# Optimization experiments

Measured on AMD Instinct MI355X. Metric: run time of the kernel, lower is better.

The kernel has to match this reference:

```python
import jax, jax.numpy as jnp
import numpy as np

N = 50000      # nodes
E = 625000     # directed edges
F_IN, H1, H2, OUT = 128, 128, 64, 50


def setup_inputs() -> dict:
    key = jax.random.key(0)
    ks = jax.random.split(key, 5)
    x = jax.random.normal(ks[0], (N, F_IN), dtype=jnp.float32)
    edge_index = jax.random.randint(ks[1], (2, E), 0, N, dtype=jnp.int64)
    W1 = jax.random.normal(ks[2], (F_IN, H1), dtype=jnp.float32) * 0.05
    b1 = jnp.zeros((H1,), jnp.float32)
    W2 = jax.random.normal(ks[3], (H1, H2), dtype=jnp.float32) * 0.05
    b2 = jnp.zeros((H2,), jnp.float32)
    Wh = jax.random.normal(ks[4], (H2, OUT), dtype=jnp.float32) * 0.05
    bh = jnp.zeros((OUT,), jnp.float32)
    return {"x": x, "edge_index": edge_index, "W1": W1, "b1": b1,
            "W2": W2, "b2": b2, "Wh": Wh, "bh": bh}


def _gcn_conv(h, W, b, src, dst, dinv, n):
    # h' = D^{-1/2} A_hat D^{-1/2} (h W) + b, A_hat includes self-loops
    h = h @ W                                   # [n, out]
    coef = (dinv[src] * dinv[dst])[:, None]      # [e, 1]
    agg = jax.ops.segment_sum(h[src] * coef, dst, num_segments=n)
    return agg + b


def reference(x, edge_index, W1, b1, W2, b2, Wh, bh):
    n = x.shape[0]
    loops = jnp.arange(n, dtype=edge_index.dtype)
    src = jnp.concatenate([edge_index[0], loops])
    dst = jnp.concatenate([edge_index[1], loops])
    # symmetric GCN normalization: deg over destinations (incl. self-loops)
    deg = jax.ops.segment_sum(jnp.ones(src.shape[0], x.dtype), dst, num_segments=n)
    dinv = jnp.where(deg > 0, jax.lax.rsqrt(deg), 0.0)
    # dropout is a no-op in eval mode (training=False)
    h = _gcn_conv(x, W1, b1, src, dst, dinv, n)
    h = jax.nn.relu(h)
    h = _gcn_conv(h, W2, b2, src, dst, dinv, n)
    h = jax.nn.relu(h)
    return h @ Wh + bh
```

## Files before the change

### kernel.cpp

```cpp
#include <hip/hip_runtime.h>

#define F_IN 128
#define HH1 128
#define HH2 64
#define FOUT 50
#define EB 256
#define NBUCK_MAX 256

typedef __attribute__((ext_vector_type(8))) short short8;
typedef __attribute__((ext_vector_type(4))) short s16x4;
typedef __attribute__((ext_vector_type(4))) float f32x4;

__device__ inline short f2bf(float f) {
    union { float f; unsigned u; } v; v.f = f;
    unsigned r = v.u + 0x7fffu + ((v.u >> 16) & 1u);
    return (short)(r >> 16);
}
__device__ inline float bf2f(short s) {
    union { float f; unsigned u; } v; v.u = ((unsigned)(unsigned short)s) << 16;
    return v.f;
}

__device__ inline int detect64(const unsigned* raw) {
    __shared__ int s_is64;
    if (threadIdx.x == 0) s_is64 = 1;
    __syncthreads();
    if (raw[2 * threadIdx.x + 1] != 0u) atomicAnd(&s_is64, 0);
    __syncthreads();
    return s_is64;
}

__global__ __launch_bounds__(256) void bucket_count(
    const int* __restrict__ raw, int E, int nbuck, int* __restrict__ parthist,
    const float* __restrict__ W1, const float* __restrict__ W2,
    const float* __restrict__ Wh, short* __restrict__ W1t,
    short* __restrict__ W2t, short* __restrict__ Wht) {
    __shared__ int hist[NBUCK_MAX];
    const int tid = threadIdx.x;
    int is64 = detect64((const unsigned*)raw);
    for (int k = tid; k < nbuck; k += 256) hist[k] = 0;
    __syncthreads();
    const int CH = (E + EB - 1) / EB;
    const int e0 = blockIdx.x * CH, e1 = min(E, e0 + CH);
    for (int e = e0 + tid; e < e1; e += 256) {
        int d = is64 ? raw[2 * (long)E + 2 * e] : raw[E + e];
        atomicAdd(&hist[d >> 8], 1);
    }
    __syncthreads();
    for (int k = tid; k < nbuck; k += 256) parthist[blockIdx.x * nbuck + k] = hist[k];
    const int T1 = HH1 * F_IN, T2 = HH2 * HH1, T3 = 64 * HH2;
    int idx = blockIdx.x * 256 + tid;
    if (idx < T1) {
        int c = idx / F_IN, k = idx - c * F_IN;
        W1t[idx] = f2bf(W1[(long)k * HH1 + c]);
    } else if (idx < T1 + T2) {
        int i = idx - T1;
        int c = i / HH1, k = i - c * HH1;
        W2t[i] = f2bf(W2[(long)k * HH2 + c]);
    } else if (idx < T1 + T2 + T3) {
        int i = idx - T1 - T2;
        int c = i / HH2, k = i - c * HH2;
        Wht[i] = f2bf((c < FOUT) ? Wh[(long)k * FOUT + c] : 0.f);
    }
}

__global__ __launch_bounds__(256) void bucket_scan(
    int* __restrict__ parthist, int* __restrict__ bbase, int nbuck, int E) {
    __shared__ int sh[256];
    const int k = threadIdx.x;
    int sum = 0;
    if (k < nbuck)
        for (int b = 0; b < EB; ++b) sum += parthist[b * nbuck + k];
    int v = (k < nbuck) ? sum : 0;
    sh[k] = v;
    __syncthreads();
    for (int off = 1; off < 256; off <<= 1) {
        int t = (k >= off) ? sh[k - off] : 0;
        __syncthreads();
        sh[k] += t;
        __syncthreads();
    }
    int base = sh[k] - v;
    if (k < nbuck) bbase[k] = base;
    if (k == 0) bbase[nbuck] = E;
    if (k < nbuck) {
        int run = base;
        for (int b = 0; b < EB; ++b) {
            int t = parthist[b * nbuck + k];
            parthist[b * nbuck + k] = run;
            run += t;
        }
    }
}

__global__ __launch_bounds__(256) void scatter_gemm1(
    const int* __restrict__ raw, int E, int nbuck,
    const int* __restrict__ parthist, int2* __restrict__ tmp,
    const float* __restrict__ x, const short* __restrict__ W1t,
    short* __restrict__ h1, int n) {
    const int tid = threadIdx.x;
    if (blockIdx.x < EB) {
        __shared__ int cur[NBUCK_MAX];
        int is64 = detect64((const unsigned*)raw);
        for (int k = tid; k < nbuck; k += 256) cur[k] = parthist[blockIdx.x * nbuck + k];
        __syncthreads();
        const int CH = (E + EB - 1) / EB;
        const int e0 = blockIdx.x * CH, e1 = min(E, e0 + CH);
        for (int e = e0 + tid; e < e1; e += 256) {
            int s, d;
            if (is64) {
                s = raw[2 * e];
                d = raw[2 * (long)E + 2 * e];
            } else {
                s = raw[e];
                d = raw[E + e];
            }
            int pos = atomicAdd(&cur[d >> 8], 1);
            tmp[pos] = make_int2(s, d);
        }
        return;
    }
    const int bid = blockIdx.x - EB;
    const int wave = tid >> 6;
    const int lane = tid & 63;
    const int l15 = lane & 15;
    const int kg = lane >> 4;
    const int rowbase = bid * 64 + wave * 16;
    const int arow = rowbase + l15;
    constexpr int KS = F_IN / 32;

    short8 af[KS];
    if (arow < n) {
        const float* xr = x + (long)arow * F_IN + kg * 8;
#pragma unroll
        for (int ks = 0; ks < KS; ++ks) {
            float4 f0 = *(const float4*)(xr + ks * 32);
            float4 f1 = *(const float4*)(xr + ks * 32 + 4);
            short8 a;
            a[0] = f2bf(f0.x); a[1] = f2bf(f0.y); a[2] = f2bf(f0.z); a[3] = f2bf(f0.w);
            a[4] = f2bf(f1.x); a[5] = f2bf(f1.y); a[6] = f2bf(f1.z); a[7] = f2bf(f1.w);
            af[ks] = a;
        }
    } else {
#pragma unroll
        for (int ks = 0; ks < KS; ++ks) af[ks] = (short8)0;
    }
    const int crowb = rowbase + kg * 4;
#pragma unroll
    for (int ct = 0; ct < HH1 / 16; ++ct) {
        const int col = ct * 16 + l15;
        const short* wr = W1t + (long)col * F_IN + kg * 8;
        f32x4 acc = {0.f, 0.f, 0.f, 0.f};
#pragma unroll
        for (int ks = 0; ks < KS; ++ks) {
            short8 bfr = *(const short8*)(wr + ks * 32);
            acc = __builtin_amdgcn_mfma_f32_16x16x32_bf16(af[ks], bfr, acc, 0, 0, 0);
        }
#pragma unroll
        for (int j = 0; j < 4; ++j) {
            int r = crowb + j;
            if (r < n) h1[(long)r * HH1 + col] = f2bf(acc[j]);
        }
    }
}

__global__ __launch_bounds__(256) void bucket_finalize(
    const int2* __restrict__ tmp, const int* __restrict__ bbase,
    int* __restrict__ rowptr, float* __restrict__ dinv,
    int* __restrict__ csr_src, int n, int nbuck) {
    __shared__ int deg[256];
    __shared__ int cur[256];
    __shared__ int sh[256];
    const int k = blockIdx.x;
    const int tid = threadIdx.x;
    const int b0 = bbase[k], b1 = bbase[k + 1];
    deg[tid] = 0;
    __syncthreads();
    for (int e = b0 + tid; e < b1; e += 256) atomicAdd(&deg[tmp[e].y & 255], 1);
    __syncthreads();
    int v = deg[tid];
    sh[tid] = v;
    __syncthreads();
    for (int off = 1; off < 256; off <<= 1) {
        int t = (tid >= off) ? sh[tid - off] : 0;
        __syncthreads();
        sh[tid] += t;
        __syncthreads();
    }
    int excl = sh[tid] - v;
    cur[tid] = excl;
    int node = (k << 8) + tid;
    if (node < n) {
        rowptr[node] = b0 + excl;
        dinv[node] = rsqrtf((float)v + 1.0f);
    }
    if (k == 0 && tid == 0) rowptr[n] = bbase[nbuck];
    __syncthreads();
    for (int e = b0 + tid; e < b1; e += 256) {
        int2 sd = tmp[e];
        int p = atomicAdd(&cur[sd.y & 255], 1);
        csr_src[b0 + p] = sd.x;
    }
}

template <int FPL>
__device__ inline void gather1(const short* p0, float c0, float* acc) {
    if constexpr (FPL == 8) {
        short8 v0 = *(const short8*)p0;
#pragma unroll
        for (int j = 0; j < 8; ++j) acc[j] = fmaf(c0, bf2f(v0[j]), acc[j]);
    } else {
        s16x4 v0 = *(const s16x4*)p0;
#pragma unroll
        for (int j = 0; j < 4; ++j) acc[j] = fmaf(c0, bf2f(v0[j]), acc[j]);
    }
}

template <int FW, bool OUT_F32>
__global__ __launch_bounds__(256) void agg_mm(
    const short* __restrict__ h, const int* __restrict__ rowptr,
    const int* __restrict__ csr_src, const float* __restrict__ dinv,
    const float* __restrict__ bias_pre, const short* __restrict__ Wt,
    const float* __restrict__ bias_post, void* __restrict__ Yv, int n,
    int ncreal) {
    constexpr int FPL = FW / 16;
    constexpr int LDW = FW + 8;
    constexpr int KS = FW / 32;
    __shared__ short tile[16][LDW];
    const int tid = threadIdx.x;
    const int grp = tid >> 4;
    const int l16 = tid & 15;
    const int node = blockIdx.x * 16 + grp;

    float acc[FPL];
#pragma unroll
    for (int j = 0; j < FPL; ++j) acc[j] = 0.f;

    if (node < n) {
        const float di = dinv[node];
#pragma unroll
        for (int j = 0; j < FPL; ++j) acc[j] = bias_pre[l16 * FPL + j];
        gather1<FPL>(h + (long)node * FW + l16 * FPL, di * di, acc);
        int e = rowptr[node];
        const int end = rowptr[node + 1];
        for (; e + 3 < end; e += 4) {
            int s0 = csr_src[e];
            int s1 = csr_src[e + 1];
            int s2 = csr_src[e + 2];
            int s3 = csr_src[e + 3];
            const short* p0 = h + (long)s0 * FW + l16 * FPL;
            const short* p1 = h + (long)s1 * FW + l16 * FPL;
            const short* p2 = h + (long)s2 * FW + l16 * FPL;
            const short* p3 = h + (long)s3 * FW + l16 * FPL;
            float c0 = dinv[s0] * di;
            float c1 = dinv[s1] * di;
            float c2 = dinv[s2] * di;
            float c3 = dinv[s3] * di;
            if constexpr (FPL == 8) {
                short8 v0 = *(const short8*)p0;
                short8 v1 = *(const short8*)p1;
                short8 v2 = *(const short8*)p2;
                short8 v3 = *(const short8*)p3;
#pragma unroll
                for (int j = 0; j < 8; ++j) acc[j] = fmaf(c0, bf2f(v0[j]), acc[j]);
#pragma unroll
                for (int j = 0; j < 8; ++j) acc[j] = fmaf(c1, bf2f(v1[j]), acc[j]);
#pragma unroll
                for (int j = 0; j < 8; ++j) acc[j] = fmaf(c2, bf2f(v2[j]), acc[j]);
#pragma unroll
                for (int j = 0; j < 8; ++j) acc[j] = fmaf(c3, bf2f(v3[j]), acc[j]);
            } else {
                s16x4 v0 = *(const s16x4*)p0;
                s16x4 v1 = *(const s16x4*)p1;
                s16x4 v2 = *(const s16x4*)p2;
                s16x4 v3 = *(const s16x4*)p3;
#pragma unroll
                for (int j = 0; j < 4; ++j) acc[j] = fmaf(c0, bf2f(v0[j]), acc[j]);
#pragma unroll
                for (int j = 0; j < 4; ++j) acc[j] = fmaf(c1, bf2f(v1[j]), acc[j]);
#pragma unroll
                for (int j = 0; j < 4; ++j) acc[j] = fmaf(c2, bf2f(v2[j]), acc[j]);
#pragma unroll
                for (int j = 0; j < 4; ++j) acc[j] = fmaf(c3, bf2f(v3[j]), acc[j]);
            }
        }
        for (; e < end; ++e) {
            int s0 = csr_src[e];
            gather1<FPL>(h + (long)s0 * FW + l16 * FPL, dinv[s0] * di, acc);
        }
    }
    if constexpr (FPL == 8) {
        short8 o;
#pragma unroll
        for (int j = 0; j < 8; ++j) o[j] = f2bf(fmaxf(acc[j], 0.f));
        *(short8*)&tile[grp][l16 * 8] = o;
    } else {
        s16x4 o;
#pragma unroll
        for (int j = 0; j < 4; ++j) o[j] = f2bf(fmaxf(acc[j], 0.f));
        *(s16x4*)&tile[grp][l16 * 4] = o;
    }
    __syncthreads();

    const int wave = tid >> 6;
    const int lane = tid & 63;
    const int l15 = lane & 15;
    const int kg = lane >> 4;
    const int col = wave * 16 + l15;
    short8 af[KS];
#pragma unroll
    for (int ks = 0; ks < KS; ++ks)
        af[ks] = *(const short8*)&tile[l15][kg * 8 + ks * 32];
    f32x4 c2 = {0.f, 0.f, 0.f, 0.f};
    const short* wr = Wt + (long)col * FW + kg * 8;
#pragma unroll
    for (int ks = 0; ks < KS; ++ks) {
        short8 bfr = *(const short8*)(wr + ks * 32);
        c2 = __builtin_amdgcn_mfma_f32_16x16x32_bf16(af[ks], bfr, c2, 0, 0, 0);
    }
    const int rb = blockIdx.x * 16 + kg * 4;
    if (OUT_F32) {
        float* Y = (float*)Yv;
#pragma unroll
        for (int j = 0; j < 4; ++j) {
            int g = rb + j;
            if (g < n && col < ncreal)
                Y[(long)g * ncreal + col] = c2[j] + bias_post[col];
        }
    } else {
        short* Y = (short*)Yv;
#pragma unroll
        for (int j = 0; j < 4; ++j) {
            int g = rb + j;
            if (g < n) Y[(long)g * 64 + col] = f2bf(c2[j]);
        }
    }
}

static inline size_t al256(size_t x) { return (x + 255) & ~(size_t)255; }

extern "C" void kernel_launch(void* const* d_in, const int* in_sizes, int n_in,
                              void* d_out, int out_size, void* d_ws, size_t ws_size,
                              hipStream_t stream) {
    const float* x    = (const float*)d_in[0];
    const int*   eraw = (const int*)d_in[1];
    const float* W1   = (const float*)d_in[2];
    const float* b1   = (const float*)d_in[3];
    const float* W2   = (const float*)d_in[4];
    const float* b2   = (const float*)d_in[5];
    const float* Wh   = (const float*)d_in[6];
    const float* bh   = (const float*)d_in[7];
    float* out = (float*)d_out;
    const int n = in_sizes[0] / F_IN;
    const int E = in_sizes[1] / 2;
    const int nbuck = (n + 255) >> 8;

    char* p = (char*)d_ws;
    float* dinv     = (float*)p; p += al256((size_t)n * 4);
    int*   rowptr   = (int*)p;   p += al256((size_t)(n + 1) * 4);
    int*   parthist = (int*)p;   p += al256((size_t)EB * nbuck * 4);
    int*   bbase    = (int*)p;   p += al256((size_t)(nbuck + 1) * 4);
    int*   csr_src  = (int*)p;   p += al256((size_t)E * 4);
    short* W1t      = (short*)p; p += al256((size_t)HH1 * F_IN * 2);
    short* W2t      = (short*)p; p += al256((size_t)HH2 * HH1 * 2);
    short* Whtp     = (short*)p; p += al256((size_t)64 * HH2 * 2);
    int2*  tmp      = (int2*)p;  p += al256((size_t)E * 8);
    short* h1       = (short*)p; p += al256((size_t)n * HH1 * 2);
    short* h2       = (short*)p;

    dim3 blk(256);
    bucket_count<<<EB, blk, 0, stream>>>(eraw, E, nbuck, parthist, W1, W2, Wh, W1t, W2t, Whtp);
    bucket_scan<<<1, blk, 0, stream>>>(parthist, bbase, nbuck, E);
    scatter_gemm1<<<EB + (n + 63) / 64, blk, 0, stream>>>(
        eraw, E, nbuck, parthist, tmp, x, W1t, h1, n);
    bucket_finalize<<<nbuck, blk, 0, stream>>>(tmp, bbase, rowptr, dinv, csr_src, n, nbuck);

    agg_mm<HH1, false><<<(n + 15) / 16, blk, 0, stream>>>(
        h1, rowptr, csr_src, dinv, b1, W2t, nullptr, h2, n, HH2);
    agg_mm<HH2, true><<<(n + 15) / 16, blk, 0, stream>>>(
        h2, rowptr, csr_src, dinv, b2, Whtp, bh, out, n, FOUT);
}
```

Measured before the change: 121.4 us.

## Parallelize bucket prefix scan across blocks with last-block global scan

Replaces the single-block bucket scan, where each thread serially walks 256 partial histograms, with a 256-block kernel. Each block scans one bucket column in parallel and writes a per-bucket total. The last block to finish, found through an atomic counter, scans the totals to produce the bucket bases. The scatter kernel now adds the bucket base to the per-block column offset. This removes a serial latency-bound loop at the cost of an atomic counter and an extra workspace array. The counter is never reset and relies on modulo 256 across calls.

New measurement: 123.5 us. Within noise of the previous version (+1.7%).

```diff
diff --git a/kernel.cpp b/kernel.cpp
--- a/kernel.cpp
+++ b/kernel.cpp
@@ -64,45 +64,56 @@
     }
 }
 
-__global__ __launch_bounds__(256) void bucket_scan(
-    int* __restrict__ parthist, int* __restrict__ bbase, int nbuck, int E) {
+__global__ __launch_bounds__(256) void scan_cols(
+    int* __restrict__ parthist, int* __restrict__ totals, int* __restrict__ bbase,
+    unsigned* __restrict__ done, int nbuck, int E) {
+    const int k = blockIdx.x;
+    const int t = threadIdx.x;
     __shared__ int sh[256];
-    const int k = threadIdx.x;
-    int sum = 0;
-    if (k < nbuck)
-        for (int b = 0; b < EB; ++b) sum += parthist[b * nbuck + k];
-    int v = (k < nbuck) ? sum : 0;
-    sh[k] = v;
+    int v = 0;
+    if (k < nbuck) v = parthist[t * nbuck + k];
+    sh[t] = v;
     __syncthreads();
     for (int off = 1; off < 256; off <<= 1) {
-        int t = (k >= off) ? sh[k - off] : 0;
-        __syncthreads();
-        sh[k] += t;
-        __syncthreads();
-    }
-    int base = sh[k] - v;
-    if (k < nbuck) bbase[k] = base;
-    if (k == 0) bbase[nbuck] = E;
-    if (k < nbuck) {
-        int run = base;
-        for (int b = 0; b < EB; ++b) {
-            int t = parthist[b * nbuck + k];
-            parthist[b * nbuck + k] = run;
-            run += t;
-        }
-    }
+        int tv = (t >= off) ? sh[t - off] : 0;
+        __syncthreads();
+        sh[t] += tv;
+        __syncthreads();
+    }
+    if (k < nbuck) parthist[t * nbuck + k] = sh[t] - v;
+    if (t == 255) totals[k] = (k < nbuck) ? sh[255] : 0;
+    __threadfence();
+    __syncthreads();
+    __shared__ unsigned s_old;
+    if (t == 0) s_old = atomicAdd(done, 1u);
+    __syncthreads();
+    if (s_old % 256u != 255u) return;
+    __threadfence();
+    int tv2 = totals[t];
+    sh[t] = tv2;
+    __syncthreads();
+    for (int off = 1; off < 256; off <<= 1) {
+        int tt = (t >= off) ? sh[t - off] : 0;
+        __syncthreads();
+        sh[t] += tt;
+        __syncthreads();
+    }
+    if (t < nbuck) bbase[t] = sh[t] - tv2;
+    if (t == 0) bbase[nbuck] = E;
 }
 
 __global__ __launch_bounds__(256) void scatter_gemm1(
     const int* __restrict__ raw, int E, int nbuck,
-    const int* __restrict__ parthist, int2* __restrict__ tmp,
+    const int* __restrict__ parthist, const int* __restrict__ bbase,
+    int2* __restrict__ tmp,
     const float* __restrict__ x, const short* __restrict__ W1t,
     short* __restrict__ h1, int n) {
     const int tid = threadIdx.x;
     if (blockIdx.x < EB) {
         __shared__ int cur[NBUCK_MAX];
         int is64 = detect64((const unsigned*)raw);
-        for (int k = tid; k < nbuck; k += 256) cur[k] = parthist[blockIdx.x * nbuck + k];
+        for (int k = tid; k < nbuck; k += 256)
+            cur[k] = bbase[k] + parthist[blockIdx.x * nbuck + k];
         __syncthreads();
         const int CH = (E + EB - 1) / EB;
         const int e0 = blockIdx.x * CH, e1 = min(E, e0 + CH);
@@ -356,9 +367,11 @@
     const int nbuck = (n + 255) >> 8;
 
     char* p = (char*)d_ws;
+    unsigned* done  = (unsigned*)p; p += 256;
     float* dinv     = (float*)p; p += al256((size_t)n * 4);
     int*   rowptr   = (int*)p;   p += al256((size_t)(n + 1) * 4);
     int*   parthist = (int*)p;   p += al256((size_t)EB * nbuck * 4);
+    int*   totals   = (int*)p;   p += al256((size_t)NBUCK_MAX * 4);
     int*   bbase    = (int*)p;   p += al256((size_t)(nbuck + 1) * 4);
     int*   csr_src  = (int*)p;   p += al256((size_t)E * 4);
     short* W1t      = (short*)p; p += al256((size_t)HH1 * F_IN * 2);
@@ -369,10 +382,11 @@
     short* h2       = (short*)p;
 
     dim3 blk(256);
-    bucket_count<<<EB, blk, 0, stream>>>(eraw, E, nbuck, parthist, W1, W2, Wh, W1t, W2t, Whtp);
-    bucket_scan<<<1, blk, 0, stream>>>(parthist, bbase, nbuck, E);
+    bucket_count<<<EB, blk, 0, stream>>>(eraw, E, nbuck, parthist,
+                                         W1, W2, Wh, W1t, W2t, Whtp);
+    scan_cols<<<NBUCK_MAX, blk, 0, stream>>>(parthist, totals, bbase, done, nbuck, E);
     scatter_gemm1<<<EB + (n + 63) / 64, blk, 0, stream>>>(
-        eraw, E, nbuck, parthist, tmp, x, W1t, h1, n);
+        eraw, E, nbuck, parthist, bbase, tmp, x, W1t, h1, n);
     bucket_finalize<<<nbuck, blk, 0, stream>>>(tmp, bbase, rowptr, dinv, csr_src, n, nbuck);
 
     agg_mm<HH1, false><<<(n + 15) / 16, blk, 0, stream>>>(
```
